# Performance work log

Hardware: AMD Instinct MI355X
Metric: run time of the kernel (lower is better)

The kernel has to match this reference:

```python
import jax, jax.numpy as jnp
import numpy as np

NEG_SLOPE = 0.01  # nn.LeakyReLU default used as CustomGCN activation

N_PAPER, N_SNAP, D = 300000, 10000, 128
E_PAPER, E_SNAP, K = 1500000, 100000, 2


def gcn(x_src, src, dst, n_dst, W, b):
    # dgl GraphConv(norm='right', in==out): aggregate src feats at dst,
    # divide by in-degree, then linear; CustomGCN applies LeakyReLU.
    msg = jax.ops.segment_sum(x_src[src], dst, num_segments=n_dst)
    deg = jax.ops.segment_sum(jnp.ones((src.shape[0],), x_src.dtype), dst, num_segments=n_dst)
    msg = msg / jnp.clip(deg, 1.0)[:, None]
    return jax.nn.leaky_relu(msg @ W + b, NEG_SLOPE)


def setup_inputs() -> dict:
    key = jax.random.key(0)
    ks = jax.random.split(key, 24)
    s = 0.05
    inp = {
        'x_paper': jax.random.normal(ks[0], (N_PAPER, D), jnp.float32),
        'x_snap': jax.random.normal(ks[1], (N_SNAP, D), jnp.float32),
        'src_pf': jax.random.randint(ks[2], (E_PAPER,), 0, N_PAPER),
        'dst_pf': jax.random.randint(ks[3], (E_PAPER,), 0, N_PAPER),
        'src_pb': jax.random.randint(ks[4], (E_PAPER,), 0, N_PAPER),
        'dst_pb': jax.random.randint(ks[5], (E_PAPER,), 0, N_PAPER),
        'src_sf': jax.random.randint(ks[6], (E_SNAP,), 0, N_SNAP),
        'dst_sf': jax.random.randint(ks[7], (E_SNAP,), 0, N_SNAP),
        'src_sb': jax.random.randint(ks[8], (E_SNAP,), 0, N_SNAP),
        'dst_sb': jax.random.randint(ks[9], (E_SNAP,), 0, N_SNAP),
        'Wp_f': jax.random.normal(ks[10], (K, D, D), jnp.float32) * s,
        'bp_f': jnp.zeros((K, D), jnp.float32),
        'Ws_f': jax.random.normal(ks[11], (K, D, D), jnp.float32) * s,
        'bs_f': jnp.zeros((K, D), jnp.float32),
        'Wp_b': jax.random.normal(ks[12], (K, D, D), jnp.float32) * s,
        'bp_b': jnp.zeros((K, D), jnp.float32),
        'Ws_b': jax.random.normal(ks[13], (K, D, D), jnp.float32) * s,
        'bs_b': jnp.zeros((K, D), jnp.float32),
        'Wc_p': jax.random.normal(ks[14], (K, 2 * D, D), jnp.float32) * s,
        'bc_p': jnp.zeros((K, D), jnp.float32),
        'Wc_s': jax.random.normal(ks[15], (K, 2 * D, D), jnp.float32) * s,
        'bc_s': jnp.zeros((K, D), jnp.float32),
    }
    return inp


def reference(x_paper, x_snap, src_pf, dst_pf, src_pb, dst_pb, src_sf, dst_sf,
              src_sb, dst_sb, Wp_f, bp_f, Ws_f, bs_f, Wp_b, bp_b, Ws_b, bs_b,
              Wc_p, bc_p, Wc_s, bc_s):
    n_p, n_s = x_paper.shape[0], x_snap.shape[0]
    hp, hs = x_paper, x_snap
    for i in range(Wp_f.shape[0]):
        # forward-direction SimpleDirectedCTSGCNLayer: inter-paper conv then snapshot conv
        fp = gcn(hp, src_pf, dst_pf, n_p, Wp_f[i], bp_f[i])
        fs = gcn(hs, src_sf, dst_sf, n_s, Ws_f[i], bs_f[i])
        # backward-direction layer on reversed edge types
        bp = gcn(hp, src_pb, dst_pb, n_p, Wp_b[i], bp_b[i])
        bs = gcn(hs, src_sb, dst_sb, n_s, Ws_b[i], bs_b[i])
        # concat_fc: per-ntype HeteroLinear(2h -> h)
        hp = jnp.concatenate([fp, bp], axis=-1) @ Wc_p[i] + bc_p[i]
        hs = jnp.concatenate([fs, bs], axis=-1) @ Wc_s[i] + bc_s[i]
    return hp, hs
```

## Files before the change

kernel.cpp:

```cpp
#include <hip/hip_runtime.h>
#include <stdint.h>

#define DF 128

typedef __attribute__((ext_vector_type(8))) short bf16x8;
typedef __attribute__((ext_vector_type(4))) float f32x4;

__device__ __forceinline__ float bf2f(uint32_t b){ union{uint32_t u; float f;} c; c.u = b<<16; return c.f; }
__device__ __forceinline__ uint16_t f2bf(float f){
  union{float f; uint32_t u;} c; c.f = f;
  return (uint16_t)((c.u + 0x7fffu + ((c.u>>16)&1u))>>16);
}

__global__ __launch_bounds__(256) void k_zero(int* __restrict__ p, int n){
  int i = blockIdx.x*256 + threadIdx.x;
  if (i < n) p[i] = 0;
}

__global__ __launch_bounds__(256) void k_count_all(
    const int* __restrict__ d0, const int* __restrict__ d1,
    const int* __restrict__ d2, const int* __restrict__ d3,
    int* __restrict__ deg, int Ep, int Es, int A1, int A2, int A3){
  int Etot = 2*Ep + 2*Es;
  for (int e = blockIdx.x*256 + threadIdx.x; e < Etot; e += gridDim.x*256){
    if (e < Ep)            atomicAdd(&deg[d0[e]], 1);
    else if (e < 2*Ep)     atomicAdd(&deg[A1 + d1[e-Ep]], 1);
    else if (e < 2*Ep+Es)  atomicAdd(&deg[A2 + d2[e-2*Ep]], 1);
    else                   atomicAdd(&deg[A3 + d3[e-2*Ep-Es]], 1);
  }
}

__global__ __launch_bounds__(256) void k_scan1(const int* __restrict__ in, int* __restrict__ out,
                                               int* __restrict__ bsum, int n){
  __shared__ int lds[256];
  int t = threadIdx.x;
  int base = blockIdx.x*1024 + t*4;
  int v0 = (base+0<n)?in[base+0]:0, v1 = (base+1<n)?in[base+1]:0;
  int v2 = (base+2<n)?in[base+2]:0, v3 = (base+3<n)?in[base+3]:0;
  int ts = v0+v1+v2+v3;
  lds[t] = ts; __syncthreads();
  for (int off=1; off<256; off<<=1){
    int x = (t>=off)?lds[t-off]:0; __syncthreads();
    lds[t] += x; __syncthreads();
  }
  int incl = lds[t];
  if (t==255) bsum[blockIdx.x] = incl;
  int run = incl - ts;
  if (base+0<n) out[base+0]=run; run+=v0;
  if (base+1<n) out[base+1]=run; run+=v1;
  if (base+2<n) out[base+2]=run; run+=v2;
  if (base+3<n) out[base+3]=run;
}

__global__ __launch_bounds__(256) void k_scan2(int* __restrict__ s, int nb){
  __shared__ int lds[256];
  __shared__ int carry;
  int t = threadIdx.x;
  if (t==0) carry = 0;
  __syncthreads();
  for (int b0=0; b0<nb; b0+=1024){
    int base = b0 + t*4;
    int v0 = (base+0<nb)?s[base+0]:0, v1 = (base+1<nb)?s[base+1]:0;
    int v2 = (base+2<nb)?s[base+2]:0, v3 = (base+3<nb)?s[base+3]:0;
    int ts = v0+v1+v2+v3;
    lds[t] = ts; __syncthreads();
    for (int off=1; off<256; off<<=1){
      int x = (t>=off)?lds[t-off]:0; __syncthreads();
      lds[t] += x; __syncthreads();
    }
    int incl = lds[t];
    int tot  = lds[255];
    int c0   = carry;
    __syncthreads();
    int run = incl - ts + c0;
    if (base+0<nb) s[base+0]=run; run+=v0;
    if (base+1<nb) s[base+1]=run; run+=v1;
    if (base+2<nb) s[base+2]=run; run+=v2;
    if (base+3<nb) s[base+3]=run;
    if (t==0) carry = c0 + tot;
    __syncthreads();
  }
}

__global__ __launch_bounds__(256) void k_add_all(int* __restrict__ rp, int* __restrict__ cur,
                                                 const int* __restrict__ bsum,
                                                 int A1, int A2, int A3,
                                                 int B1, int B2, int B3, int NT){
  int i = blockIdx.x*256 + threadIdx.x;
  if (i >= NT) return;
  int b = (i < A1) ? 0 : (i < A2) ? B1 : (i < A3) ? B2 : B3;
  int v = rp[i] + bsum[i>>10] - b;
  rp[i] = v; cur[i] = v;
}

__global__ __launch_bounds__(256) void k_fill_all(
    const int* __restrict__ s0, const int* __restrict__ d0,
    const int* __restrict__ s1, const int* __restrict__ d1,
    const int* __restrict__ s2, const int* __restrict__ d2,
    const int* __restrict__ s3, const int* __restrict__ d3,
    int* __restrict__ cur,
    int* __restrict__ c0, int* __restrict__ c1, int* __restrict__ c2, int* __restrict__ c3,
    int Ep, int Es, int A1, int A2, int A3){
  int Etot = 2*Ep + 2*Es;
  for (int e = blockIdx.x*256 + threadIdx.x; e < Etot; e += gridDim.x*256){
    if (e < Ep){            int p = atomicAdd(&cur[d0[e]], 1);                 c0[p] = s0[e]; }
    else if (e < 2*Ep){     int q = e-Ep;      int p = atomicAdd(&cur[A1+d1[q]], 1); c1[p] = s1[q]; }
    else if (e < 2*Ep+Es){  int q = e-2*Ep;    int p = atomicAdd(&cur[A2+d2[q]], 1); c2[p] = s2[q]; }
    else{                   int q = e-2*Ep-Es; int p = atomicAdd(&cur[A3+d3[q]], 1); c3[p] = s3[q]; }
  }
}

__global__ __launch_bounds__(256) void k_cast(const float* __restrict__ xp, const float* __restrict__ xs,
                                              uint16_t* __restrict__ hp, uint16_t* __restrict__ hs,
                                              int npE, int total4){
  int i = blockIdx.x*256 + threadIdx.x;
  if (i >= total4) return;
  int e = i*4;
  const float* src; uint16_t* dst; int o;
  if (e < npE){ src = xp; dst = hp; o = e; }
  else        { src = xs; dst = hs; o = e - npE; }
  float4 v = *(const float4*)(src + o);
  ushort4 u;
  u.x = f2bf(v.x); u.y = f2bf(v.y); u.z = f2bf(v.z); u.w = f2bf(v.w);
  *(ushort4*)(dst + o) = u;
}

__global__ __launch_bounds__(256) void k_transpose_all(
    const float* __restrict__ Wpf, const float* __restrict__ Wpb,
    const float* __restrict__ Wsf, const float* __restrict__ Wsb,
    const float* __restrict__ Wcp, const float* __restrict__ Wcs,
    uint16_t* __restrict__ wt, int K){
  int idx = blockIdx.x*256 + threadIdx.x;
  if (idx >= K*8*16384) return;
  int ls = idx >> 14, layer = ls >> 3, slot = ls & 7;
  int within = idx & 16383, n = within >> 7, k = within & 127;
  const float* src; int kOff = 0;
  switch (slot){
    case 0: src = Wpf + (size_t)layer*16384; break;
    case 1: src = Wpb + (size_t)layer*16384; break;
    case 2: src = Wsf + (size_t)layer*16384; break;
    case 3: src = Wsb + (size_t)layer*16384; break;
    case 4: src = Wcp + (size_t)layer*32768; break;
    case 5: src = Wcp + (size_t)layer*32768; kOff = 128; break;
    case 6: src = Wcs + (size_t)layer*32768; break;
    default: src = Wcs + (size_t)layer*32768; kOff = 128; break;
  }
  wt[idx] = f2bf(src[(size_t)(kOff + k)*DF + n]);
}

__global__ __launch_bounds__(256) void k_agg_all(
    const uint16_t* __restrict__ hp, const uint16_t* __restrict__ hs,
    const int* __restrict__ rpAll, int A1, int A2, int A3,
    const int* __restrict__ c0, const int* __restrict__ c1,
    const int* __restrict__ c2, const int* __restrict__ c3,
    uint16_t* __restrict__ o0, uint16_t* __restrict__ o1,
    uint16_t* __restrict__ o2, uint16_t* __restrict__ o3,
    int Np, int Ns, int gp, int gs){
  int b = blockIdx.x, w = threadIdx.x >> 6, lane = threadIdx.x & 63;
  const uint16_t* x; const int* rp; const int* col; uint16_t* out; int n, row;
  if (b < gp)            { x=hp; rp=rpAll;    col=c0; out=o0; n=Np; row=b*4+w; }
  else if (b < 2*gp)     { x=hp; rp=rpAll+A1; col=c1; out=o1; n=Np; row=(b-gp)*4+w; }
  else if (b < 2*gp+gs)  { x=hs; rp=rpAll+A2; col=c2; out=o2; n=Ns; row=(b-2*gp)*4+w; }
  else                   { x=hs; rp=rpAll+A3; col=c3; out=o3; n=Ns; row=(b-2*gp-gs)*4+w; }
  if (row >= n) return;
  int beg = rp[row], end = rp[row+1];
  int deg = end - beg;
  int cidx = beg + lane;
  int cl = (cidx < end) ? col[cidx] : 0;
  int dd = (deg > 64) ? 64 : deg;
  float a0=0.f,a1=0.f,b0=0.f,b1=0.f,cc0=0.f,cc1=0.f,d0=0.f,d1=0.f;
  int e = 0;
  for (; e+3 < dd; e += 4){
    int s0 = __shfl(cl, e),   s1 = __shfl(cl, e+1);
    int s2 = __shfl(cl, e+2), s3 = __shfl(cl, e+3);
    uint32_t u0 = *(const uint32_t*)(x + ((size_t)s0<<7) + (lane<<1));
    uint32_t u1 = *(const uint32_t*)(x + ((size_t)s1<<7) + (lane<<1));
    uint32_t u2 = *(const uint32_t*)(x + ((size_t)s2<<7) + (lane<<1));
    uint32_t u3 = *(const uint32_t*)(x + ((size_t)s3<<7) + (lane<<1));
    a0  += bf2f(u0 & 0xffffu); a1  += bf2f(u0 >> 16);
    b0  += bf2f(u1 & 0xffffu); b1  += bf2f(u1 >> 16);
    cc0 += bf2f(u2 & 0xffffu); cc1 += bf2f(u2 >> 16);
    d0  += bf2f(u3 & 0xffffu); d1  += bf2f(u3 >> 16);
  }
  for (; e < dd; ++e){
    int s0 = __shfl(cl, e);
    uint32_t u0 = *(const uint32_t*)(x + ((size_t)s0<<7) + (lane<<1));
    a0 += bf2f(u0 & 0xffffu); a1 += bf2f(u0 >> 16);
  }
  if (deg > 64){
    for (int e2 = beg+64; e2 < end; ++e2){
      int s = col[e2];
      uint32_t u = *(const uint32_t*)(x + ((size_t)s<<7) + (lane<<1));
      a0 += bf2f(u & 0xffffu); a1 += bf2f(u >> 16);
    }
  }
  float s0f = (a0+b0)+(cc0+d0), s1f = (a1+b1)+(cc1+d1);
  float inv = 1.0f / fmaxf((float)deg, 1.0f);
  uint32_t pk = (uint32_t)f2bf(s0f*inv) | ((uint32_t)f2bf(s1f*inv) << 16);
  *(uint32_t*)(out + ((size_t)row<<7) + (lane<<1)) = pk;
}

__device__ __forceinline__ void stageA(uint16_t (*sA)[128], const uint16_t* __restrict__ Ap,
                                       int m0, int M, int t){
#pragma unroll
  for (int i=0;i<4;++i){
    int c = t + i*256, r = c>>4, ch = c&15;
    int gr = m0 + r;
    uint4 val = {0u,0u,0u,0u};
    if (gr < M) val = *(const uint4*)(Ap + (size_t)gr*DF + (ch<<3));
    *(uint4*)(&sA[r][(ch ^ (r&7))<<3]) = val;
  }
}
__device__ __forceinline__ void stageW(uint16_t (*sW)[128], const uint16_t* __restrict__ Wp, int t){
#pragma unroll
  for (int i=0;i<8;++i){
    int c = t + i*256, r = c>>4, ch = c&15;
    *(uint4*)(&sW[r][(ch ^ (r&7))<<3]) = *(const uint4*)(Wp + (size_t)r*DF + (ch<<3));
  }
}
__device__ __forceinline__ void mfma_pass(const uint16_t (*sA)[128], const uint16_t (*sW)[128],
                                          f32x4* acc, int w, int lane){
  int ar = (w<<4) + (lane&15);
  int q  = lane>>4;
#pragma unroll
  for (int kc=0;kc<4;++kc){
    int ch = kc*4 + q;
    bf16x8 afrag = *(const bf16x8*)(&sA[ar][(ch ^ (ar&7))<<3]);
#pragma unroll
    for (int n=0;n<8;++n){
      int br = (n<<4)+(lane&15);
      bf16x8 bfrag = *(const bf16x8*)(&sW[br][(ch ^ (br&7))<<3]);
      acc[n] = __builtin_amdgcn_mfma_f32_16x16x32_bf16(afrag, bfrag, acc[n], 0, 0, 0);
    }
  }
}
__device__ __forceinline__ void store_act_lds(uint16_t (*sA)[128], const f32x4* acc,
                                              const float* __restrict__ bias, int w, int lane){
#pragma unroll
  for (int n=0;n<8;++n){
    int cv = (n<<4) + (lane&15);
    float bv = bias[cv];
#pragma unroll
    for (int r=0;r<4;++r){
      int lr = (w<<4) + ((lane>>4)<<2) + r;
      float v = acc[n][r] + bv;
      v = (v > 0.f) ? v : 0.01f*v;
      sA[lr][(((cv>>3) ^ (lr&7))<<3) + (cv&7)] = f2bf(v);
    }
  }
}

template<int OUTF32>
__global__ __launch_bounds__(256) void k_layer(
    const uint16_t* __restrict__ Afp, const uint16_t* __restrict__ Abp,
    const uint16_t* __restrict__ Afs, const uint16_t* __restrict__ Abs,
    const uint16_t* __restrict__ wtl,
    const float* __restrict__ bpf, const float* __restrict__ bpb, const float* __restrict__ bcp,
    const float* __restrict__ bsf, const float* __restrict__ bsb, const float* __restrict__ bcs,
    uint16_t* __restrict__ hpb, uint16_t* __restrict__ hsb,
    float* __restrict__ outP, float* __restrict__ outS,
    int Np, int Ns, int bp){
  __shared__ uint16_t sF[64][128];
  __shared__ uint16_t sB[64][128];
  __shared__ uint16_t sW[128][128];
  int b = blockIdx.x, t = threadIdx.x, w = t>>6, lane = t&63;
  const uint16_t *Af,*Ab,*wf,*wb,*wct,*wcb; const float *bf_,*bb_,*bc_;
  uint16_t* hb; float* of; int M, lb;
  if (b < bp){
    Af=Afp; Ab=Abp; wf=wtl; wb=wtl+16384; wct=wtl+4*16384; wcb=wtl+5*16384;
    bf_=bpf; bb_=bpb; bc_=bcp; hb=hpb; of=outP; M=Np; lb=b;
  } else {
    Af=Afs; Ab=Abs; wf=wtl+2*16384; wb=wtl+3*16384; wct=wtl+6*16384; wcb=wtl+7*16384;
    bf_=bsf; bb_=bsb; bc_=bcs; hb=hsb; of=outS; M=Ns; lb=b-bp;
  }
  int m0 = lb*64;

  f32x4 accF[8], accB[8], accC[8];
#pragma unroll
  for (int n=0;n<8;++n){ accF[n]=(f32x4){0,0,0,0}; accB[n]=(f32x4){0,0,0,0}; accC[n]=(f32x4){0,0,0,0}; }

  stageA(sF, Af, m0, M, t);
  stageA(sB, Ab, m0, M, t);
  stageW(sW, wf, t);
  __syncthreads();
  mfma_pass(sF, sW, accF, w, lane);
  __syncthreads();
  stageW(sW, wb, t);
  __syncthreads();
  mfma_pass(sB, sW, accB, w, lane);
  store_act_lds(sF, accF, bf_, w, lane);
  store_act_lds(sB, accB, bb_, w, lane);
  __syncthreads();
  stageW(sW, wct, t);
  __syncthreads();
  mfma_pass(sF, sW, accC, w, lane);
  __syncthreads();
  stageW(sW, wcb, t);
  __syncthreads();
  mfma_pass(sB, sW, accC, w, lane);

#pragma unroll
  for (int n=0;n<8;++n){
    int cv = (n<<4)+(lane&15);
    float bv = bc_[cv];
#pragma unroll
    for (int r=0;r<4;++r){
      int lr = (w<<4)+((lane>>4)<<2)+r;
      int grow = m0 + lr;
      if (grow < M){
        float v = accC[n][r] + bv;
        if (OUTF32) of[(size_t)grow*DF + cv] = v;
        else        hb[(size_t)grow*DF + cv] = f2bf(v);
      }
    }
  }
}

extern "C" void kernel_launch(void* const* d_in, const int* in_sizes, int n_in,
                              void* d_out, int out_size, void* d_ws, size_t ws_size,
                              hipStream_t stream){
  const float* x_paper = (const float*)d_in[0];
  const float* x_snap  = (const float*)d_in[1];
  const int* src_pf = (const int*)d_in[2]; const int* dst_pf = (const int*)d_in[3];
  const int* src_pb = (const int*)d_in[4]; const int* dst_pb = (const int*)d_in[5];
  const int* src_sf = (const int*)d_in[6]; const int* dst_sf = (const int*)d_in[7];
  const int* src_sb = (const int*)d_in[8]; const int* dst_sb = (const int*)d_in[9];
  const float* Wpf = (const float*)d_in[10]; const float* bpf = (const float*)d_in[11];
  const float* Wsf = (const float*)d_in[12]; const float* bsf = (const float*)d_in[13];
  const float* Wpb = (const float*)d_in[14]; const float* bpb = (const float*)d_in[15];
  const float* Wsb = (const float*)d_in[16]; const float* bsb = (const float*)d_in[17];
  const float* Wcp = (const float*)d_in[18]; const float* bcp = (const float*)d_in[19];
  const float* Wcs = (const float*)d_in[20]; const float* bcs = (const float*)d_in[21];

  const int Np = in_sizes[0]/DF, Ns = in_sizes[1]/DF;
  const int Ep = in_sizes[2],    Es = in_sizes[6];
  const int K  = in_sizes[10]/(DF*DF);

  const int P1 = ((Np + 1 + 1023)/1024)*1024;
  const int Ps = ((Ns + 1 + 1023)/1024)*1024;
  const int A1 = P1, A2 = 2*P1, A3 = 2*P1 + Ps, NT = 2*P1 + 2*Ps;
  const int B1 = Ep, B2 = 2*Ep, B3 = 2*Ep + Es;

  uint8_t* base = (uint8_t*)d_ws;
  size_t off = 0;
  auto carve = [&](size_t bytes)->void*{
    void* p = base + off;
    off = (off + bytes + 255) & ~(size_t)255;
    return p;
  };

  int* degAll = (int*)carve((size_t)NT*4);
  int* rpAll  = (int*)carve((size_t)NT*4);
  int* curAll = (int*)carve((size_t)NT*4);
  int* bsum   = (int*)carve(4096*4);
  int* col0 = (int*)carve((size_t)Ep*4);
  int* col1 = (int*)carve((size_t)Ep*4);
  int* col2 = (int*)carve((size_t)Es*4);
  int* col3 = (int*)carve((size_t)Es*4);
  uint16_t* wt   = (uint16_t*)carve((size_t)K*8*16384*2);
  uint16_t* hp_b = (uint16_t*)carve((size_t)Np*DF*2);
  uint16_t* hs_b = (uint16_t*)carve((size_t)Ns*DF*2);
  uint16_t* Afp  = (uint16_t*)carve((size_t)Np*DF*2);
  uint16_t* Abp  = (uint16_t*)carve((size_t)Np*DF*2);
  uint16_t* Afs  = (uint16_t*)carve((size_t)Ns*DF*2);
  uint16_t* Abs  = (uint16_t*)carve((size_t)Ns*DF*2);

  const int Etot = 2*Ep + 2*Es;
  int eblk = (Etot + 255)/256; if (eblk > 2048) eblk = 2048;

  k_zero<<<(NT+255)/256, 256, 0, stream>>>(degAll, NT);
  k_count_all<<<eblk, 256, 0, stream>>>(dst_pf, dst_pb, dst_sf, dst_sb, degAll, Ep, Es, A1, A2, A3);
  k_scan1<<<NT/1024, 256, 0, stream>>>(degAll, rpAll, bsum, NT);
  k_scan2<<<1, 256, 0, stream>>>(bsum, NT/1024);
  k_add_all<<<(NT+255)/256, 256, 0, stream>>>(rpAll, curAll, bsum, A1, A2, A3, B1, B2, B3, NT);
  k_fill_all<<<eblk, 256, 0, stream>>>(src_pf, dst_pf, src_pb, dst_pb, src_sf, dst_sf, src_sb, dst_sb,
                                       curAll, col0, col1, col2, col3, Ep, Es, A1, A2, A3);

  const int npE = Np*DF, total4 = (Np + Ns)*DF/4;
  k_cast<<<(total4+255)/256, 256, 0, stream>>>(x_paper, x_snap, hp_b, hs_b, npE, total4);
  k_transpose_all<<<(K*8*16384+255)/256, 256, 0, stream>>>(Wpf, Wpb, Wsf, Wsb, Wcp, Wcs, wt, K);

  float* outP = (float*)d_out;
  float* outS = outP + (size_t)Np*DF;
  const int gp = (Np+3)/4, gs = (Ns+3)/4;
  const int bp = (Np+63)/64, bs = (Ns+63)/64;

  for (int i=0; i<K; ++i){
    const uint16_t* wtl = wt + (size_t)i*8*16384;
    k_agg_all<<<2*gp + 2*gs, 256, 0, stream>>>(hp_b, hs_b, rpAll, A1, A2, A3,
                                               col0, col1, col2, col3,
                                               Afp, Abp, Afs, Abs, Np, Ns, gp, gs);
    if (i == K-1)
      k_layer<1><<<bp + bs, 256, 0, stream>>>(Afp, Abp, Afs, Abs, wtl,
                                              bpf + (size_t)i*DF, bpb + (size_t)i*DF, bcp + (size_t)i*DF,
                                              bsf + (size_t)i*DF, bsb + (size_t)i*DF, bcs + (size_t)i*DF,
                                              hp_b, hs_b, outP, outS, Np, Ns, bp);
    else
      k_layer<0><<<bp + bs, 256, 0, stream>>>(Afp, Abp, Afs, Abs, wtl,
                                              bpf + (size_t)i*DF, bpb + (size_t)i*DF, bcp + (size_t)i*DF,
                                              bsf + (size_t)i*DF, bsb + (size_t)i*DF, bcs + (size_t)i*DF,
                                              hp_b, hs_b, outP, outS, Np, Ns, bp);
  }
}
```

Measured before the change: 1.375 ms.

## Partition CSR build atomics by destination window per XCD

```diff
diff --git a/kernel.cpp b/kernel.cpp
--- a/kernel.cpp
+++ b/kernel.cpp
@@ -17,16 +17,22 @@
   if (i < n) p[i] = 0;
 }
 
-__global__ __launch_bounds__(256) void k_count_all(
+__global__ __launch_bounds__(256) void k_count_allw(
     const int* __restrict__ d0, const int* __restrict__ d1,
     const int* __restrict__ d2, const int* __restrict__ d3,
-    int* __restrict__ deg, int Ep, int Es, int A1, int A2, int A3){
+    int* __restrict__ deg, int Ep, int Es, int A1, int A2, int A3,
+    int wp, int wsn){
+  int g  = blockIdx.x & 7;
+  int T  = (gridDim.x >> 3) * 256;
+  int tid = (blockIdx.x >> 3)*256 + threadIdx.x;
+  int plo = g*wp,  phi = plo + wp;
+  int slo = g*wsn, shi = slo + wsn;
   int Etot = 2*Ep + 2*Es;
-  for (int e = blockIdx.x*256 + threadIdx.x; e < Etot; e += gridDim.x*256){
-    if (e < Ep)            atomicAdd(&deg[d0[e]], 1);
-    else if (e < 2*Ep)     atomicAdd(&deg[A1 + d1[e-Ep]], 1);
-    else if (e < 2*Ep+Es)  atomicAdd(&deg[A2 + d2[e-2*Ep]], 1);
-    else                   atomicAdd(&deg[A3 + d3[e-2*Ep-Es]], 1);
+  for (int e = tid; e < Etot; e += T){
+    if (e < Ep){           int d = d0[e];          if (d>=plo && d<phi) atomicAdd(&deg[d], 1); }
+    else if (e < 2*Ep){    int d = d1[e-Ep];       if (d>=plo && d<phi) atomicAdd(&deg[A1+d], 1); }
+    else if (e < 2*Ep+Es){ int d = d2[e-2*Ep];     if (d>=slo && d<shi) atomicAdd(&deg[A2+d], 1); }
+    else{                  int d = d3[e-2*Ep-Es];  if (d>=slo && d<shi) atomicAdd(&deg[A3+d], 1); }
   }
 }
 
@@ -93,20 +99,34 @@
   rp[i] = v; cur[i] = v;
 }
 
-__global__ __launch_bounds__(256) void k_fill_all(
+__global__ __launch_bounds__(256) void k_fill_allw(
     const int* __restrict__ s0, const int* __restrict__ d0,
     const int* __restrict__ s1, const int* __restrict__ d1,
     const int* __restrict__ s2, const int* __restrict__ d2,
     const int* __restrict__ s3, const int* __restrict__ d3,
     int* __restrict__ cur,
     int* __restrict__ c0, int* __restrict__ c1, int* __restrict__ c2, int* __restrict__ c3,
-    int Ep, int Es, int A1, int A2, int A3){
+    int Ep, int Es, int A1, int A2, int A3, int wp, int wsn){
+  int g  = blockIdx.x & 7;
+  int T  = (gridDim.x >> 3) * 256;
+  int tid = (blockIdx.x >> 3)*256 + threadIdx.x;
+  int plo = g*wp,  phi = plo + wp;
+  int slo = g*wsn, shi = slo + wsn;
   int Etot = 2*Ep + 2*Es;
-  for (int e = blockIdx.x*256 + threadIdx.x; e < Etot; e += gridDim.x*256){
-    if (e < Ep){            int p = atomicAdd(&cur[d0[e]], 1);                 c0[p] = s0[e]; }
-    else if (e < 2*Ep){     int q = e-Ep;      int p = atomicAdd(&cur[A1+d1[q]], 1); c1[p] = s1[q]; }
-    else if (e < 2*Ep+Es){  int q = e-2*Ep;    int p = atomicAdd(&cur[A2+d2[q]], 1); c2[p] = s2[q]; }
-    else{                   int q = e-2*Ep-Es; int p = atomicAdd(&cur[A3+d3[q]], 1); c3[p] = s3[q]; }
+  for (int e = tid; e < Etot; e += T){
+    if (e < Ep){
+      int d = d0[e];
+      if (d>=plo && d<phi){ int p = atomicAdd(&cur[d], 1); c0[p] = s0[e]; }
+    } else if (e < 2*Ep){
+      int q = e-Ep; int d = d1[q];
+      if (d>=plo && d<phi){ int p = atomicAdd(&cur[A1+d], 1); c1[p] = s1[q]; }
+    } else if (e < 2*Ep+Es){
+      int q = e-2*Ep; int d = d2[q];
+      if (d>=slo && d<shi){ int p = atomicAdd(&cur[A2+d], 1); c2[p] = s2[q]; }
+    } else {
+      int q = e-2*Ep-Es; int d = d3[q];
+      if (d>=slo && d<shi){ int p = atomicAdd(&cur[A3+d], 1); c3[p] = s3[q]; }
+    }
   }
 }
 
@@ -340,6 +360,8 @@
   const int Ps = ((Ns + 1 + 1023)/1024)*1024;
   const int A1 = P1, A2 = 2*P1, A3 = 2*P1 + Ps, NT = 2*P1 + 2*Ps;
   const int B1 = Ep, B2 = 2*Ep, B3 = 2*Ep + Es;
+  const int wp  = (Np + 7)/8;
+  const int wsn = (Ns + 7)/8;
 
   uint8_t* base = (uint8_t*)d_ws;
   size_t off = 0;
@@ -365,16 +387,14 @@
   uint16_t* Afs  = (uint16_t*)carve((size_t)Ns*DF*2);
   uint16_t* Abs  = (uint16_t*)carve((size_t)Ns*DF*2);
 
-  const int Etot = 2*Ep + 2*Es;
-  int eblk = (Etot + 255)/256; if (eblk > 2048) eblk = 2048;
-
   k_zero<<<(NT+255)/256, 256, 0, stream>>>(degAll, NT);
-  k_count_all<<<eblk, 256, 0, stream>>>(dst_pf, dst_pb, dst_sf, dst_sb, degAll, Ep, Es, A1, A2, A3);
+  k_count_allw<<<2048, 256, 0, stream>>>(dst_pf, dst_pb, dst_sf, dst_sb, degAll,
+                                         Ep, Es, A1, A2, A3, wp, wsn);
   k_scan1<<<NT/1024, 256, 0, stream>>>(degAll, rpAll, bsum, NT);
   k_scan2<<<1, 256, 0, stream>>>(bsum, NT/1024);
   k_add_all<<<(NT+255)/256, 256, 0, stream>>>(rpAll, curAll, bsum, A1, A2, A3, B1, B2, B3, NT);
-  k_fill_all<<<eblk, 256, 0, stream>>>(src_pf, dst_pf, src_pb, dst_pb, src_sf, dst_sf, src_sb, dst_sb,
-                                       curAll, col0, col1, col2, col3, Ep, Es, A1, A2, A3);
+  k_fill_allw<<<2048, 256, 0, stream>>>(src_pf, dst_pf, src_pb, dst_pb, src_sf, dst_sf, src_sb, dst_sb,
+                                        curAll, col0, col1, col2, col3, Ep, Es, A1, A2, A3, wp, wsn);
 
   const int npE = Np*DF, total4 = (Np + Ns)*DF/4;
   k_cast<<<(total4+255)/256, 256, 0, stream>>>(x_paper, x_snap, hp_b, hs_b, npE, total4);
```

Result: faster. 1.265 ms (-8.0%).
